# Optimization experiments

Hardware: AMD Instinct MI355X
Metric: run time of the kernel (lower is better)

The kernel has to match this reference:

```python
import jax, jax.numpy as jnp
import numpy as np

B, S, D = 4, 4096, 64

def setup_inputs() -> dict:
    key = jax.random.key(0)
    k1, k2, k3 = jax.random.split(key, 3)
    inputs = jax.random.normal(k1, (B, S, D), dtype=jnp.float32)
    rotation = jax.random.normal(k2, (D, D), dtype=jnp.float32)
    entangle = jax.random.normal(k3, (D, D), dtype=jnp.float32)
    return {"inputs": inputs, "rotation": rotation, "entangle": entangle}

def reference(inputs, rotation, entangle):
    # query/key projections: [B,S,D] @ [D,D] -> [B,S,D]
    query = jnp.einsum('bsd,de->bse', inputs, rotation)
    key = jnp.einsum('bsd,de->bse', inputs, entangle)
    scale = 1.0 / jnp.sqrt(jnp.float32(inputs.shape[-1]))
    # scores: [B,S,S] softmax over last axis
    scores = jax.nn.softmax(jnp.einsum('bqd,bkd->bqk', query, key) * scale, axis=-1)
    # values are the raw inputs (no value projection)
    return jnp.einsum('bqk,bkd->bqd', scores, inputs)
```

## Files before the change

### kernel.cpp

```cpp
#include <hip/hip_runtime.h>
#include <hip/hip_fp16.h>

#define BB 4
#define SS 4096
#define DD 64
#define NSPLIT 4
#define KT_PER (SS / 64 / NSPLIT)

typedef _Float16 half8 __attribute__((ext_vector_type(8)));
typedef _Float16 half4 __attribute__((ext_vector_type(4)));
typedef __fp16 fp16x2 __attribute__((ext_vector_type(2)));
typedef float floatx4 __attribute__((ext_vector_type(4)));

__global__ __launch_bounds__(256) void proj_kernel(
    const float* __restrict__ X, const float* __restrict__ R, const float* __restrict__ E,
    _Float16* __restrict__ Qhi, _Float16* __restrict__ Qlo,
    _Float16* __restrict__ Khi, _Float16* __restrict__ Klo,
    _Float16* __restrict__ Vt)
{
    __shared__ float Rs[64][64];
    __shared__ float Es[64][64];
    __shared__ float Xs[16][68];
    int t = threadIdx.x;
    long rowbase = (long)blockIdx.x * 16;

    for (int j = 0; j < 4; ++j) {
        int idx = j * 256 + t;
        int r = idx >> 4;
        int c = (idx & 15) * 4;
        *(float4*)&Rs[r][c] = ((const float4*)R)[idx];
        *(float4*)&Es[r][c] = ((const float4*)E)[idx];
    }
    *(float4*)&Xs[t >> 4][(t & 15) * 4] = ((const float4*)(X + rowbase * 64))[t];
    __syncthreads();

    int row = t >> 4;
    int c0 = (t & 15) * 4;
    float q[4] = {0.f, 0.f, 0.f, 0.f}, k[4] = {0.f, 0.f, 0.f, 0.f};
#pragma unroll 4
    for (int d = 0; d < 64; ++d) {
        float x = Xs[row][d];
        float4 rv = *(const float4*)&Rs[d][c0];
        float4 ev = *(const float4*)&Es[d][c0];
        q[0] = fmaf(x, rv.x, q[0]); q[1] = fmaf(x, rv.y, q[1]);
        q[2] = fmaf(x, rv.z, q[2]); q[3] = fmaf(x, rv.w, q[3]);
        k[0] = fmaf(x, ev.x, k[0]); k[1] = fmaf(x, ev.y, k[1]);
        k[2] = fmaf(x, ev.z, k[2]); k[3] = fmaf(x, ev.w, k[3]);
    }
    long gq = (rowbase + row) * 64 + c0;
    half4 qh, ql, kh, kl;
#pragma unroll
    for (int j = 0; j < 4; ++j) {
        _Float16 h = (_Float16)q[j];
        qh[j] = h; ql[j] = (_Float16)(q[j] - (float)h);
        h = (_Float16)k[j];
        kh[j] = h; kl[j] = (_Float16)(k[j] - (float)h);
    }
    *(half4*)(Qhi + gq) = qh; *(half4*)(Qlo + gq) = ql;
    *(half4*)(Khi + gq) = kh; *(half4*)(Klo + gq) = kl;

    int d = t >> 2;
    int si = (t & 3) * 4;
    int b = (int)(rowbase >> 12);
    int sbase = (int)(rowbase & 4095);
    half4 v;
#pragma unroll
    for (int j = 0; j < 4; ++j) v[j] = (_Float16)Xs[si + j][d];
    *(half4*)(Vt + ((long)(b * 64 + d)) * SS + sbase + si) = v;
}

#define L2E 1.44269504088896340736f

__device__ __forceinline__ void glds16(const _Float16* g, _Float16* l) {
    __builtin_amdgcn_global_load_lds(
        (const __attribute__((address_space(1))) unsigned*)g,
        (__attribute__((address_space(3))) unsigned*)l, 16, 0, 0);
}

__global__ __launch_bounds__(128, 2) void attn_partial(
    const _Float16* __restrict__ Qhi, const _Float16* __restrict__ Qlo,
    const _Float16* __restrict__ Khi, const _Float16* __restrict__ Klo,
    const _Float16* __restrict__ Vt,
    float* __restrict__ Op, float* __restrict__ Mp, float* __restrict__ Lp)
{
    __shared__ _Float16 Ksh[2][64 * 64];
    __shared__ _Float16 Ksl[2][64 * 64];
    __shared__ _Float16 Ps[2 * 32 * 64];

    int t = threadIdx.x;
    int wave = t >> 6;
    int lane = t & 63;
    int l15 = lane & 15;
    int quad = lane >> 4;
    int split = blockIdx.y;
    int b = blockIdx.z;
    int q0 = blockIdx.x * 64 + wave * 32;

    half8 qah0, qah1, qbh0, qbh1, qal0, qal1, qbl0, qbl1;
    {
        long qrow = ((long)b * SS + q0 + l15) * DD;
        qah0 = *(const half8*)(Qhi + qrow + quad * 8);
        qah1 = *(const half8*)(Qhi + qrow + 32 + quad * 8);
        qal0 = *(const half8*)(Qlo + qrow + quad * 8);
        qal1 = *(const half8*)(Qlo + qrow + 32 + quad * 8);
        long qrow2 = qrow + 16 * DD;
        qbh0 = *(const half8*)(Qhi + qrow2 + quad * 8);
        qbh1 = *(const half8*)(Qhi + qrow2 + 32 + quad * 8);
        qbl0 = *(const half8*)(Qlo + qrow2 + quad * 8);
        qbl1 = *(const half8*)(Qlo + qrow2 + 32 + quad * 8);
    }

    floatx4 o[2][4];
#pragma unroll
    for (int qh = 0; qh < 2; ++qh)
#pragma unroll
        for (int i = 0; i < 4; ++i) o[qh][i] = (floatx4){0.f, 0.f, 0.f, 0.f};
    float m_q[2] = {-1e30f, -1e30f};
    float l_q[2] = {0.f, 0.f};

    const float scale = 0.125f * L2E;

    int grow = lane >> 3;
    int gblk = (lane & 7) ^ grow;
    int rm = l15 & 7;
    int p0h = ((quad ^ rm) << 3);

    int kt0 = split * KT_PER;
    const _Float16* khs_base = Khi + ((long)b * SS + (long)kt0 * 64) * DD;
    const _Float16* kls_base = Klo + ((long)b * SS + (long)kt0 * 64) * DD;

#pragma unroll
    for (int j = 0; j < 4; ++j) {
        int c = wave * 4 + j;
        long goff = (long)(c * 8 + grow) * 64 + gblk * 8;
        glds16(khs_base + goff, &Ksh[0][c * 512]);
        glds16(kls_base + goff, &Ksl[0][c * 512]);
    }

    for (int i = 0; i < KT_PER; ++i) {
        int kt = kt0 + i;
        int buf = i & 1;
        __syncthreads();

        half8 vb[4][2];
#pragma unroll
        for (int dt = 0; dt < 4; ++dt)
#pragma unroll
            for (int h = 0; h < 2; ++h)
                vb[dt][h] = *(const half8*)(Vt + ((long)(b * 64 + dt * 16 + l15)) * SS
                                            + kt * 64 + h * 32 + quad * 8);

        if (i + 1 < KT_PER) {
            long tbase = (long)(i + 1) * 64 * DD;
#pragma unroll
            for (int j = 0; j < 4; ++j) {
                int c = wave * 4 + j;
                long goff = tbase + (long)(c * 8 + grow) * 64 + gblk * 8;
                glds16(khs_base + goff, &Ksh[buf ^ 1][c * 512]);
                glds16(kls_base + goff, &Ksl[buf ^ 1][c * 512]);
            }
        }

        floatx4 s[2][4];
#pragma unroll
        for (int ct = 0; ct < 4; ++ct) {
            int rowb = (ct * 16 + l15) * 64;
            half8 ka0h = *(const half8*)&Ksh[buf][rowb + p0h];
            half8 ka1h = *(const half8*)&Ksh[buf][rowb + (p0h ^ 32)];
            half8 ka0l = *(const half8*)&Ksl[buf][rowb + p0h];
            half8 ka1l = *(const half8*)&Ksl[buf][rowb + (p0h ^ 32)];
            floatx4 acc0 = {0.f, 0.f, 0.f, 0.f};
            acc0 = __builtin_amdgcn_mfma_f32_16x16x32_f16(ka0h, qah0, acc0, 0, 0, 0);
            acc0 = __builtin_amdgcn_mfma_f32_16x16x32_f16(ka1h, qah1, acc0, 0, 0, 0);
            acc0 = __builtin_amdgcn_mfma_f32_16x16x32_f16(ka0h, qal0, acc0, 0, 0, 0);
            acc0 = __builtin_amdgcn_mfma_f32_16x16x32_f16(ka1h, qal1, acc0, 0, 0, 0);
            acc0 = __builtin_amdgcn_mfma_f32_16x16x32_f16(ka0l, qah0, acc0, 0, 0, 0);
            acc0 = __builtin_amdgcn_mfma_f32_16x16x32_f16(ka1l, qah1, acc0, 0, 0, 0);
            s[0][ct] = acc0;
            floatx4 acc1 = {0.f, 0.f, 0.f, 0.f};
            acc1 = __builtin_amdgcn_mfma_f32_16x16x32_f16(ka0h, qbh0, acc1, 0, 0, 0);
            acc1 = __builtin_amdgcn_mfma_f32_16x16x32_f16(ka1h, qbh1, acc1, 0, 0, 0);
            acc1 = __builtin_amdgcn_mfma_f32_16x16x32_f16(ka0h, qbl0, acc1, 0, 0, 0);
            acc1 = __builtin_amdgcn_mfma_f32_16x16x32_f16(ka1h, qbl1, acc1, 0, 0, 0);
            acc1 = __builtin_amdgcn_mfma_f32_16x16x32_f16(ka0l, qbh0, acc1, 0, 0, 0);
            acc1 = __builtin_amdgcn_mfma_f32_16x16x32_f16(ka1l, qbh1, acc1, 0, 0, 0);
            s[1][ct] = acc1;
        }

#pragma unroll
        for (int qh = 0; qh < 2; ++qh) {
            float mt = s[qh][0][0];
#pragma unroll
            for (int ct = 0; ct < 4; ++ct)
#pragma unroll
                for (int r = 0; r < 4; ++r)
                    mt = fmaxf(mt, s[qh][ct][r]);
            mt = fmaxf(mt, __shfl_xor(mt, 16));
            mt = fmaxf(mt, __shfl_xor(mt, 32));
            mt *= scale;
            float mn = fmaxf(m_q[qh], mt);
            float alpha = exp2f(m_q[qh] - mn);
            m_q[qh] = mn;

            int prow = (wave * 32 + qh * 16 + l15) * 64;
            float rs = 0.f;
#pragma unroll
            for (int ct = 0; ct < 4; ++ct) {
                float p0 = exp2f(s[qh][ct][0] * scale - mn);
                float p1 = exp2f(s[qh][ct][1] * scale - mn);
                float p2 = exp2f(s[qh][ct][2] * scale - mn);
                float p3 = exp2f(s[qh][ct][3] * scale - mn);
                rs += (p0 + p1) + (p2 + p3);
                union { fp16x2 h2[2]; half4 h4; } u;
                u.h2[0] = __builtin_amdgcn_cvt_pkrtz(p0, p1);
                u.h2[1] = __builtin_amdgcn_cvt_pkrtz(p2, p3);
                int blk = (2 * ct + (quad >> 1)) ^ rm;
                *(half4*)&Ps[prow + blk * 8 + (quad & 1) * 4] = u.h4;
            }
            rs += __shfl_xor(rs, 16);
            rs += __shfl_xor(rs, 32);
            l_q[qh] = l_q[qh] * alpha + rs;

#pragma unroll
            for (int r = 0; r < 4; ++r) {
                float a = __shfl(alpha, quad * 4 + r);
                o[qh][0][r] *= a; o[qh][1][r] *= a;
                o[qh][2][r] *= a; o[qh][3][r] *= a;
            }
        }

#pragma unroll
        for (int h = 0; h < 2; ++h) {
            int pblk = ((4 * h + quad) ^ rm) << 3;
            half8 pa0 = *(const half8*)&Ps[(wave * 32 + l15) * 64 + pblk];
            half8 pa1 = *(const half8*)&Ps[(wave * 32 + 16 + l15) * 64 + pblk];
#pragma unroll
            for (int dt = 0; dt < 4; ++dt) {
                o[0][dt] = __builtin_amdgcn_mfma_f32_16x16x32_f16(pa0, vb[dt][h], o[0][dt], 0, 0, 0);
                o[1][dt] = __builtin_amdgcn_mfma_f32_16x16x32_f16(pa1, vb[dt][h], o[1][dt], 0, 0, 0);
            }
        }
    }

    long pbase = ((long)b * NSPLIT + split) * SS;
#pragma unroll
    for (int qh = 0; qh < 2; ++qh) {
#pragma unroll
        for (int r = 0; r < 4; ++r) {
            int q = q0 + qh * 16 + quad * 4 + r;
            long orow = (pbase + q) * DD;
#pragma unroll
            for (int dt = 0; dt < 4; ++dt)
                Op[orow + dt * 16 + l15] = o[qh][dt][r];
        }
    }
    if (quad == 0) {
        Mp[pbase + q0 + l15] = m_q[0];
        Lp[pbase + q0 + l15] = l_q[0];
        Mp[pbase + q0 + 16 + l15] = m_q[1];
        Lp[pbase + q0 + 16 + l15] = l_q[1];
    }
}

__global__ __launch_bounds__(256) void combine_kernel(
    const float* __restrict__ Op, const float* __restrict__ Mp,
    const float* __restrict__ Lp, float* __restrict__ Out)
{
    int t = threadIdx.x;
    int qi = t >> 4;
    int d4 = (t & 15) * 4;
    long gq = (long)blockIdx.x * 16 + qi;
    int b = (int)(gq >> 12);
    int s = (int)(gq & 4095);

    float m = -1e30f;
    for (int i = 0; i < NSPLIT; ++i)
        m = fmaxf(m, Mp[((long)b * NSPLIT + i) * SS + s]);
    float l = 0.f;
    float4 o = {0.f, 0.f, 0.f, 0.f};
    for (int i = 0; i < NSPLIT; ++i) {
        long pb = ((long)b * NSPLIT + i) * SS + s;
        float a = exp2f(Mp[pb] - m);
        l = fmaf(Lp[pb], a, l);
        float4 oi = *(const float4*)(Op + pb * DD + d4);
        o.x = fmaf(oi.x, a, o.x); o.y = fmaf(oi.y, a, o.y);
        o.z = fmaf(oi.z, a, o.z); o.w = fmaf(oi.w, a, o.w);
    }
    float inv = 1.f / l;
    float4 r = {o.x * inv, o.y * inv, o.z * inv, o.w * inv};
    *(float4*)(Out + gq * DD + d4) = r;
}

extern "C" void kernel_launch(void* const* d_in, const int* in_sizes, int n_in,
                              void* d_out, int out_size, void* d_ws, size_t ws_size,
                              hipStream_t stream) {
    const float* X = (const float*)d_in[0];
    const float* R = (const float*)d_in[1];
    const float* E = (const float*)d_in[2];
    float* Out = (float*)d_out;

    const size_t N = (size_t)BB * SS * DD;
    _Float16* Qhi = (_Float16*)d_ws;
    _Float16* Qlo = Qhi + N;
    _Float16* Khi = Qlo + N;
    _Float16* Klo = Khi + N;
    _Float16* Vt  = Klo + N;
    float* Op = (float*)(Vt + N);
    float* Mp = Op + (size_t)BB * NSPLIT * SS * DD;
    float* Lp = Mp + (size_t)BB * NSPLIT * SS;

    proj_kernel<<<dim3(BB * SS / 16), 256, 0, stream>>>(X, R, E, Qhi, Qlo, Khi, Klo, Vt);
    attn_partial<<<dim3(SS / 64, NSPLIT, BB), 128, 0, stream>>>(Qhi, Qlo, Khi, Klo, Vt, Op, Mp, Lp);
    combine_kernel<<<dim3(BB * SS / 16), 256, 0, stream>>>(Op, Mp, Lp, Out);
}
```

Before: 125.1 us.

## Double per-wave query rows and compute row sums via MFMA with ones

```diff
diff --git a/kernel.cpp b/kernel.cpp
--- a/kernel.cpp
+++ b/kernel.cpp
@@ -77,7 +77,7 @@
         (__attribute__((address_space(3))) unsigned*)l, 16, 0, 0);
 }
 
-__global__ __launch_bounds__(128, 2) void attn_partial(
+__global__ __launch_bounds__(128) void attn_partial(
     const _Float16* __restrict__ Qhi, const _Float16* __restrict__ Qlo,
     const _Float16* __restrict__ Khi, const _Float16* __restrict__ Klo,
     const _Float16* __restrict__ Vt,
@@ -85,7 +85,7 @@
 {
     __shared__ _Float16 Ksh[2][64 * 64];
     __shared__ _Float16 Ksl[2][64 * 64];
-    __shared__ _Float16 Ps[2 * 32 * 64];
+    __shared__ _Float16 Ps[2 * 64 * 64];
 
     int t = threadIdx.x;
     int wave = t >> 6;
@@ -94,31 +94,32 @@
     int quad = lane >> 4;
     int split = blockIdx.y;
     int b = blockIdx.z;
-    int q0 = blockIdx.x * 64 + wave * 32;
-
-    half8 qah0, qah1, qbh0, qbh1, qal0, qal1, qbl0, qbl1;
-    {
-        long qrow = ((long)b * SS + q0 + l15) * DD;
-        qah0 = *(const half8*)(Qhi + qrow + quad * 8);
-        qah1 = *(const half8*)(Qhi + qrow + 32 + quad * 8);
-        qal0 = *(const half8*)(Qlo + qrow + quad * 8);
-        qal1 = *(const half8*)(Qlo + qrow + 32 + quad * 8);
-        long qrow2 = qrow + 16 * DD;
-        qbh0 = *(const half8*)(Qhi + qrow2 + quad * 8);
-        qbh1 = *(const half8*)(Qhi + qrow2 + 32 + quad * 8);
-        qbl0 = *(const half8*)(Qlo + qrow2 + quad * 8);
-        qbl1 = *(const half8*)(Qlo + qrow2 + 32 + quad * 8);
-    }
-
-    floatx4 o[2][4];
-#pragma unroll
-    for (int qh = 0; qh < 2; ++qh)
-#pragma unroll
-        for (int i = 0; i < 4; ++i) o[qh][i] = (floatx4){0.f, 0.f, 0.f, 0.f};
-    float m_q[2] = {-1e30f, -1e30f};
-    float l_q[2] = {0.f, 0.f};
+    int q0 = blockIdx.x * 128 + wave * 64;
+
+    half8 qfh[4][2], qfl[4][2];
+#pragma unroll
+    for (int g = 0; g < 4; ++g) {
+        long qrow = ((long)b * SS + q0 + g * 16 + l15) * DD;
+        qfh[g][0] = *(const half8*)(Qhi + qrow + quad * 8);
+        qfh[g][1] = *(const half8*)(Qhi + qrow + 32 + quad * 8);
+        qfl[g][0] = *(const half8*)(Qlo + qrow + quad * 8);
+        qfl[g][1] = *(const half8*)(Qlo + qrow + 32 + quad * 8);
+    }
+
+    floatx4 o[4][4];
+    floatx4 ol[4];
+#pragma unroll
+    for (int g = 0; g < 4; ++g) {
+        ol[g] = (floatx4){0.f, 0.f, 0.f, 0.f};
+#pragma unroll
+        for (int i = 0; i < 4; ++i) o[g][i] = (floatx4){0.f, 0.f, 0.f, 0.f};
+    }
+    float m_q[4] = {-1e30f, -1e30f, -1e30f, -1e30f};
 
     const float scale = 0.125f * L2E;
+    half8 ones8;
+#pragma unroll
+    for (int j = 0; j < 8; ++j) ones8[j] = (_Float16)1.0f;
 
     int grow = lane >> 3;
     int gblk = (lane & 7) ^ grow;
@@ -161,7 +162,7 @@
             }
         }
 
-        floatx4 s[2][4];
+        floatx4 s[4][4];
 #pragma unroll
         for (int ct = 0; ct < 4; ++ct) {
             int rowb = (ct * 16 + l15) * 64;
@@ -169,97 +170,96 @@
             half8 ka1h = *(const half8*)&Ksh[buf][rowb + (p0h ^ 32)];
             half8 ka0l = *(const half8*)&Ksl[buf][rowb + p0h];
             half8 ka1l = *(const half8*)&Ksl[buf][rowb + (p0h ^ 32)];
-            floatx4 acc0 = {0.f, 0.f, 0.f, 0.f};
-            acc0 = __builtin_amdgcn_mfma_f32_16x16x32_f16(ka0h, qah0, acc0, 0, 0, 0);
-            acc0 = __builtin_amdgcn_mfma_f32_16x16x32_f16(ka1h, qah1, acc0, 0, 0, 0);
-            acc0 = __builtin_amdgcn_mfma_f32_16x16x32_f16(ka0h, qal0, acc0, 0, 0, 0);
-            acc0 = __builtin_amdgcn_mfma_f32_16x16x32_f16(ka1h, qal1, acc0, 0, 0, 0);
-            acc0 = __builtin_amdgcn_mfma_f32_16x16x32_f16(ka0l, qah0, acc0, 0, 0, 0);
-            acc0 = __builtin_amdgcn_mfma_f32_16x16x32_f16(ka1l, qah1, acc0, 0, 0, 0);
-            s[0][ct] = acc0;
-            floatx4 acc1 = {0.f, 0.f, 0.f, 0.f};
-            acc1 = __builtin_amdgcn_mfma_f32_16x16x32_f16(ka0h, qbh0, acc1, 0, 0, 0);
-            acc1 = __builtin_amdgcn_mfma_f32_16x16x32_f16(ka1h, qbh1, acc1, 0, 0, 0);
-            acc1 = __builtin_amdgcn_mfma_f32_16x16x32_f16(ka0h, qbl0, acc1, 0, 0, 0);
-            acc1 = __builtin_amdgcn_mfma_f32_16x16x32_f16(ka1h, qbl1, acc1, 0, 0, 0);
-            acc1 = __builtin_amdgcn_mfma_f32_16x16x32_f16(ka0l, qbh0, acc1, 0, 0, 0);
-            acc1 = __builtin_amdgcn_mfma_f32_16x16x32_f16(ka1l, qbh1, acc1, 0, 0, 0);
-            s[1][ct] = acc1;
-        }
-
-#pragma unroll
-        for (int qh = 0; qh < 2; ++qh) {
-            float mt = s[qh][0][0];
+#pragma unroll
+            for (int g = 0; g < 4; ++g) {
+                floatx4 acc = {0.f, 0.f, 0.f, 0.f};
+                acc = __builtin_amdgcn_mfma_f32_16x16x32_f16(ka0h, qfh[g][0], acc, 0, 0, 0);
+                acc = __builtin_amdgcn_mfma_f32_16x16x32_f16(ka1h, qfh[g][1], acc, 0, 0, 0);
+                acc = __builtin_amdgcn_mfma_f32_16x16x32_f16(ka0h, qfl[g][0], acc, 0, 0, 0);
+                acc = __builtin_amdgcn_mfma_f32_16x16x32_f16(ka1h, qfl[g][1], acc, 0, 0, 0);
+                acc = __builtin_amdgcn_mfma_f32_16x16x32_f16(ka0l, qfh[g][0], acc, 0, 0, 0);
+                acc = __builtin_amdgcn_mfma_f32_16x16x32_f16(ka1l, qfh[g][1], acc, 0, 0, 0);
+                s[g][ct] = acc;
+            }
+        }
+
+#pragma unroll
+        for (int g = 0; g < 4; ++g) {
+            float mt = s[g][0][0];
 #pragma unroll
             for (int ct = 0; ct < 4; ++ct)
 #pragma unroll
                 for (int r = 0; r < 4; ++r)
-                    mt = fmaxf(mt, s[qh][ct][r]);
+                    mt = fmaxf(mt, s[g][ct][r]);
             mt = fmaxf(mt, __shfl_xor(mt, 16));
             mt = fmaxf(mt, __shfl_xor(mt, 32));
             mt *= scale;
-            float mn = fmaxf(m_q[qh], mt);
-            float alpha = exp2f(m_q[qh] - mn);
-            m_q[qh] = mn;
-
-            int prow = (wave * 32 + qh * 16 + l15) * 64;
-            float rs = 0.f;
+            float mn = fmaxf(m_q[g], mt);
+            float alpha = exp2f(m_q[g] - mn);
+            m_q[g] = mn;
+
+            int prow = (wave * 64 + g * 16 + l15) * 64;
 #pragma unroll
             for (int ct = 0; ct < 4; ++ct) {
-                float p0 = exp2f(s[qh][ct][0] * scale - mn);
-                float p1 = exp2f(s[qh][ct][1] * scale - mn);
-                float p2 = exp2f(s[qh][ct][2] * scale - mn);
-                float p3 = exp2f(s[qh][ct][3] * scale - mn);
-                rs += (p0 + p1) + (p2 + p3);
+                float p0 = exp2f(s[g][ct][0] * scale - mn);
+                float p1 = exp2f(s[g][ct][1] * scale - mn);
+                float p2 = exp2f(s[g][ct][2] * scale - mn);
+                float p3 = exp2f(s[g][ct][3] * scale - mn);
                 union { fp16x2 h2[2]; half4 h4; } u;
                 u.h2[0] = __builtin_amdgcn_cvt_pkrtz(p0, p1);
                 u.h2[1] = __builtin_amdgcn_cvt_pkrtz(p2, p3);
                 int blk = (2 * ct + (quad >> 1)) ^ rm;
                 *(half4*)&Ps[prow + blk * 8 + (quad & 1) * 4] = u.h4;
             }
-            rs += __shfl_xor(rs, 16);
-            rs += __shfl_xor(rs, 32);
-            l_q[qh] = l_q[qh] * alpha + rs;
 
 #pragma unroll
             for (int r = 0; r < 4; ++r) {
                 float a = __shfl(alpha, quad * 4 + r);
-                o[qh][0][r] *= a; o[qh][1][r] *= a;
-                o[qh][2][r] *= a; o[qh][3][r] *= a;
+                o[g][0][r] *= a; o[g][1][r] *= a;
+                o[g][2][r] *= a; o[g][3][r] *= a;
+                ol[g][r] *= a;
             }
         }
 
 #pragma unroll
         for (int h = 0; h < 2; ++h) {
             int pblk = ((4 * h + quad) ^ rm) << 3;
-            half8 pa0 = *(const half8*)&Ps[(wave * 32 + l15) * 64 + pblk];
-            half8 pa1 = *(const half8*)&Ps[(wave * 32 + 16 + l15) * 64 + pblk];
-#pragma unroll
-            for (int dt = 0; dt < 4; ++dt) {
-                o[0][dt] = __builtin_amdgcn_mfma_f32_16x16x32_f16(pa0, vb[dt][h], o[0][dt], 0, 0, 0);
-                o[1][dt] = __builtin_amdgcn_mfma_f32_16x16x32_f16(pa1, vb[dt][h], o[1][dt], 0, 0, 0);
+#pragma unroll
+            for (int g = 0; g < 4; ++g) {
+                half8 pa = *(const half8*)&Ps[(wave * 64 + g * 16 + l15) * 64 + pblk];
+#pragma unroll
+                for (int dt = 0; dt < 4; ++dt)
+                    o[g][dt] = __builtin_amdgcn_mfma_f32_16x16x32_f16(pa, vb[dt][h], o[g][dt], 0, 0, 0);
+                ol[g] = __builtin_amdgcn_mfma_f32_16x16x32_f16(pa, ones8, ol[g], 0, 0, 0);
             }
         }
     }
 
     long pbase = ((long)b * NSPLIT + split) * SS;
 #pragma unroll
-    for (int qh = 0; qh < 2; ++qh) {
+    for (int g = 0; g < 4; ++g) {
 #pragma unroll
         for (int r = 0; r < 4; ++r) {
-            int q = q0 + qh * 16 + quad * 4 + r;
+            int q = q0 + g * 16 + quad * 4 + r;
             long orow = (pbase + q) * DD;
 #pragma unroll
             for (int dt = 0; dt < 4; ++dt)
-                Op[orow + dt * 16 + l15] = o[qh][dt][r];
+                Op[orow + dt * 16 + l15] = o[g][dt][r];
         }
     }
     if (quad == 0) {
-        Mp[pbase + q0 + l15] = m_q[0];
-        Lp[pbase + q0 + l15] = l_q[0];
-        Mp[pbase + q0 + 16 + l15] = m_q[1];
-        Lp[pbase + q0 + 16 + l15] = l_q[1];
-    }
+#pragma unroll
+        for (int g = 0; g < 4; ++g)
+            Mp[pbase + q0 + g * 16 + l15] = m_q[g];
+    }
+    if (l15 == 0) {
+#pragma unroll
+        for (int g = 0; g < 4; ++g)
+#pragma unroll
+            for (int r = 0; r < 4; ++r)
+                Lp[pbase + q0 + g * 16 + quad * 4 + r] = ol[g][r];
+    }
+
 }
 
 __global__ __launch_bounds__(256) void combine_kernel(
@@ -310,6 +310,6 @@
     float* Lp = Mp + (size_t)BB * NSPLIT * SS;
 
     proj_kernel<<<dim3(BB * SS / 16), 256, 0, stream>>>(X, R, E, Qhi, Qlo, Khi, Klo, Vt);
-    attn_partial<<<dim3(SS / 64, NSPLIT, BB), 128, 0, stream>>>(Qhi, Qlo, Khi, Klo, Vt, Op, Mp, Lp);
+    attn_partial<<<dim3(SS / 128, NSPLIT, BB), 128, 0, stream>>>(Qhi, Qlo, Khi, Klo, Vt, Op, Mp, Lp);
     combine_kernel<<<dim3(BB * SS / 16), 256, 0, stream>>>(Op, Mp, Lp, Out);
 }
```

Result: slower. 146.0 us (+16.7%).
